# Kernel optimization log

Measured on AMD Instinct MI355X. Metric: run time of the kernel, lower is better.

## Reference

```python
import jax, jax.numpy as jnp
import numpy as np

DELAY = 4
SKIP = 2
NF = 8
HS = 256
EPS = 1e-5


def setup_inputs() -> dict:
    key = jax.random.key(0)
    ks = jax.random.split(key, 11)
    B, NP, NO, T = 16, 512, 512, 2048
    predictor = jax.random.normal(ks[0], (B, NP, T), dtype=jnp.float32)
    to_order = jax.random.normal(ks[1], (B, NO, T), dtype=jnp.float32)
    trilinear = jax.random.normal(ks[2], (NF, NO, NP), dtype=jnp.float32) / np.float32(np.sqrt(NP * NO))
    w_o = jax.random.normal(ks[3], (HS, NO), dtype=jnp.float32) / np.float32(np.sqrt(NO))
    b_o = jax.random.normal(ks[4], (HS,), dtype=jnp.float32) * 0.01
    w_p = jax.random.normal(ks[5], (HS, NP), dtype=jnp.float32) / np.float32(np.sqrt(NP))
    b_p = jax.random.normal(ks[6], (HS,), dtype=jnp.float32) * 0.01
    bn_gamma = jnp.ones((HS,), dtype=jnp.float32)
    bn_beta = jnp.zeros((HS,), dtype=jnp.float32)
    w_out = jax.random.normal(ks[7], (NF, HS), dtype=jnp.float32) / np.float32(np.sqrt(HS))
    b_out = jax.random.normal(ks[8], (NF,), dtype=jnp.float32) * 0.01
    return {"predictor": predictor, "to_order": to_order, "trilinear": trilinear,
            "w_o": w_o, "b_o": b_o, "w_p": w_p, "b_p": b_p,
            "bn_gamma": bn_gamma, "bn_beta": bn_beta, "w_out": w_out, "b_out": b_out}


def reference(predictor, to_order, trilinear, w_o, b_o, w_p, b_p, bn_gamma, bn_beta, w_out, b_out):
    B, NP, T = predictor.shape
    NO = to_order.shape[1]
    tot_latency = DELAY + SKIP * (NF - 1)
    T_r = T - tot_latency
    pred = predictor[:, :, :T_r]          # (B, np, Tr)
    too = to_order[:, :, DELAY:]          # (B, no, T - delay)
    # predictor_product[b,k,t,m] = sum_p pred[b,p,t] * trilinear[k,m,p]
    pp = jnp.einsum('bpt,kmp->bktm', pred, trilinear)           # (B, nf, Tr, no)
    win = jnp.stack([too[:, :, j * SKIP: j * SKIP + T_r] for j in range(NF)], axis=1)  # (B, nf, no, Tr)
    inner = jnp.einsum('bjmt,bktm->bjkt', win, pp)              # (B, nf, nf, Tr)
    # conv1d (kernel 1) heads
    o_proj = jnp.einsum('hm,bmt->bht', w_o, too) + b_o[None, :, None]    # (B, hs, T - delay)
    p_proj = jnp.einsum('hp,bpt->bht', w_p, pred) + b_p[None, :, None]   # (B, hs, Tr)
    o_win = jnp.stack([o_proj[:, :, j * SKIP: j * SKIP + T_r] for j in range(NF)], axis=1)  # (B, nf, hs, Tr)
    h = jax.nn.relu(o_win + p_proj[:, None])                    # (B, nf, hs, Tr)
    # BatchNorm1d (training-mode batch stats) over (B*nf, hs, Tr): stats over axes (0,1,3)
    mean = h.mean(axis=(0, 1, 3), keepdims=True)
    var = h.var(axis=(0, 1, 3), keepdims=True)
    h = (h - mean) * jax.lax.rsqrt(var + EPS) * bn_gamma[None, None, :, None] + bn_beta[None, None, :, None]
    head = jnp.einsum('kh,bjht->bjkt', w_out, h) + b_out[None, None, :, None]
    inner = inner + head
    log_probs = jax.nn.log_softmax(inner, axis=2)               # (B, nf, nf, Tr)
    correct = jnp.einsum('bjjt->bjt', log_probs)                # diagonal j == k
    return correct.mean(axis=2).mean(axis=0)                    # (nf,)
```

## Files before the change

### kernel.cpp

```cpp
#include <hip/hip_runtime.h>
#include <math.h>

constexpr int B_  = 16;
constexpr int NP_ = 512;
constexpr int NO_ = 512;
constexpr int T_  = 2048;
constexpr int NF_ = 8;
constexpr int HS_ = 256;
constexpr int TR_ = 2030;
constexpr int TO_ = 2044;
constexpr int OPLD_ = 2048;
constexpr float EPS_ = 1e-5f;

typedef short bf16x8 __attribute__((ext_vector_type(8)));
typedef float f32x16 __attribute__((ext_vector_type(16)));

__device__ __forceinline__ unsigned short f2bf(float f) {
  union { float f; unsigned int u; } v; v.f = f;
  unsigned int r = v.u + 0x7fffu + ((v.u >> 16) & 1u);
  return (unsigned short)(r >> 16);
}
__device__ __forceinline__ float bf2f(unsigned short u) {
  union { unsigned int u; float f; } v; v.u = ((unsigned int)u) << 16;
  return v.f;
}

typedef const __attribute__((address_space(1))) unsigned int* gas_u32;
typedef __attribute__((address_space(3))) unsigned int* las_u32;
__device__ __forceinline__ void gl16(const void* g, void* l) {
  __builtin_amdgcn_global_load_lds((gas_u32)g, (las_u32)l, 16, 0, 0);
}


__global__ __launch_bounds__(256) void transpose_cvt(
    const float* __restrict__ inA, unsigned short* __restrict__ outA,
    const float* __restrict__ inB, unsigned short* __restrict__ outB) {
  __shared__ float tile[64][65];
  const int c0 = blockIdx.x * 64;
  const int r0 = blockIdx.y * 64;
  const int z  = blockIdx.z;
  const int b  = z & 15;
  const float* ib = ((z < 16) ? inA : inB) + (size_t)b * 512 * 2048;
  unsigned short* ob = ((z < 16) ? outA : outB) + (size_t)b * 2048 * 512;
  for (int i = threadIdx.x; i < 64 * 16; i += 256) {
    const int r = i >> 4, c4 = (i & 15) * 4;
    float4 v = *(const float4*)(ib + (size_t)(r0 + r) * 2048 + c0 + c4);
    tile[r][c4 + 0] = v.x; tile[r][c4 + 1] = v.y;
    tile[r][c4 + 2] = v.z; tile[r][c4 + 3] = v.w;
  }
  __syncthreads();
  for (int i = threadIdx.x; i < 64 * 8; i += 256) {
    const int c = i >> 3, r8 = (i & 7) * 8;
    unsigned int pk[4];
    #pragma unroll
    for (int e = 0; e < 4; ++e)
      pk[e] = (unsigned int)f2bf(tile[r8 + 2 * e][c]) |
              ((unsigned int)f2bf(tile[r8 + 2 * e + 1][c]) << 16);
    *(uint4*)(ob + (size_t)(c0 + c) * 512 + r0 + r8) = *(uint4*)pk;
  }
}

__global__ __launch_bounds__(256) void cvt_all(
    const float* __restrict__ tri, unsigned short* __restrict__ trib,
    const float* __restrict__ wo, unsigned short* __restrict__ wob,
    const float* __restrict__ wp, unsigned short* __restrict__ wpb) {
  const int n1 = NF_ * NO_ * NP_, n2 = HS_ * 512;
  int i = (blockIdx.x * 256 + threadIdx.x) * 4;
  const float* in; unsigned short* out;
  if (i < n1)           { in = tri; out = trib; }
  else if (i < n1 + n2) { i -= n1; in = wo; out = wob; }
  else                  { i -= n1 + n2; in = wp; out = wpb; }
  float4 v = *(const float4*)(in + i);
  ushort4 o; o.x = f2bf(v.x); o.y = f2bf(v.y); o.z = f2bf(v.z); o.w = f2bf(v.w);
  *(ushort4*)(out + i) = o;
}

__global__ __launch_bounds__(256, 2) void proj_mfma(
    const unsigned short* __restrict__ Wo, const unsigned short* __restrict__ Wp,
    const unsigned short* __restrict__ Xo, const unsigned short* __restrict__ Xp,
    const float* __restrict__ biasO, const float* __restrict__ biasP,
    unsigned short* __restrict__ outO, unsigned short* __restrict__ outP) {
  __shared__ char smem[65536];
  char* const Ab[2] = { smem, smem + 16384 };
  char* const Bb[2] = { smem + 32768, smem + 49152 };
  const int sel = blockIdx.y >> 1;
  const unsigned short* Wbf = sel ? Wp : Wo;
  const unsigned short* Xt  = sel ? Xp : Xo;
  const float* bias = sel ? biasP : biasO;
  unsigned short* out = sel ? outP : outO;
  const int Tlen = sel ? TR_ : TO_;
  const int toff = sel ? 0 : 4;
  const int tid = threadIdx.x;
  const int l = tid & 63, wv = tid >> 6;
  const int h = l >> 5, tl = l & 31;
  const int mq = wv >> 1, tq = wv & 1;
  const int t0 = blockIdx.x * 128;
  const int m0 = (blockIdx.y & 1) * 128;
  const int b  = blockIdx.z;
  const unsigned short* Xb = Xt + (size_t)b * T_ * 512;

  int aSrc[4], bSrc[4], ldsO[4];
  #pragma unroll
  for (int i = 0; i < 4; ++i) {
    const int q = (wv << 8) + (i << 6) + l;
    const int r = q >> 3, c8s = (q & 7) ^ (r & 7);
    aSrc[i] = (m0 + r) * 512 + (c8s << 3);
    const int row = min(t0 + toff + r, T_ - 1);
    bSrc[i] = row * 512 + (c8s << 3);
    ldsO[i] = ((wv << 8) + (i << 6)) << 4;
  }

  f32x16 acc[2][2];
  #pragma unroll
  for (int i = 0; i < 2; ++i)
    #pragma unroll
    for (int jj = 0; jj < 2; ++jj)
      #pragma unroll
      for (int e = 0; e < 16; ++e) acc[i][jj][e] = 0.f;

  #pragma unroll
  for (int i = 0; i < 4; ++i) gl16(Wbf + aSrc[i], Ab[0] + ldsO[i]);
  #pragma unroll
  for (int i = 0; i < 4; ++i) gl16(Xb + bSrc[i], Bb[0] + ldsO[i]);
  asm volatile("s_waitcnt vmcnt(0)" ::: "memory");
  __builtin_amdgcn_s_barrier();

  #pragma unroll
  for (int ps = 0; ps < 8; ++ps) {
    const int cb = ps & 1;
    if (ps < 7) {
      const int p0 = (ps + 1) << 6;
      #pragma unroll
      for (int i = 0; i < 4; ++i) gl16(Wbf + p0 + aSrc[i], Ab[cb ^ 1] + ldsO[i]);
      #pragma unroll
      for (int i = 0; i < 4; ++i) gl16(Xb + p0 + bSrc[i], Bb[cb ^ 1] + ldsO[i]);
    }
    const unsigned short* As = (const unsigned short*)Ab[cb];
    const unsigned short* Bs = (const unsigned short*)Bb[cb];
    #pragma unroll
    for (int s = 0; s < 4; ++s) {
      const int k8 = 2 * s + h;
      bf16x8 af[2], bfr[2];
      #pragma unroll
      for (int mt = 0; mt < 2; ++mt) {
        const int rm = 64 * mq + 32 * mt + tl;
        af[mt] = *(const bf16x8*)(As + rm * 64 + ((k8 ^ (rm & 7)) << 3));
      }
      #pragma unroll
      for (int nt = 0; nt < 2; ++nt) {
        const int rt = 64 * tq + 32 * nt + tl;
        bfr[nt] = *(const bf16x8*)(Bs + rt * 64 + ((k8 ^ (rt & 7)) << 3));
      }
      #pragma unroll
      for (int mt = 0; mt < 2; ++mt)
        #pragma unroll
        for (int nt = 0; nt < 2; ++nt)
          acc[mt][nt] = __builtin_amdgcn_mfma_f32_32x32x16_bf16(
              af[mt], bfr[nt], acc[mt][nt], 0, 0, 0);
    }
    asm volatile("s_waitcnt vmcnt(0)" ::: "memory");
    __builtin_amdgcn_s_barrier();
  }
  #pragma unroll
  for (int mt = 0; mt < 2; ++mt)
    #pragma unroll
    for (int nt = 0; nt < 2; ++nt)
      #pragma unroll
      for (int r = 0; r < 16; ++r) {
        const int hs = m0 + 64 * mq + 32 * mt + (r & 3) + 8 * (r >> 2) + 4 * h;
        const int t  = t0 + 64 * tq + 32 * nt + tl;
        if (t < Tlen)
          out[((size_t)b * HS_ + hs) * OPLD_ + t] = f2bf(acc[mt][nt][r] + bias[hs]);
      }
}

__global__ __launch_bounds__(256, 2) void inner_mfma(
    const unsigned short* __restrict__ pred_t,
    const unsigned short* __restrict__ too_t,
    const unsigned short* __restrict__ tri_bf,
    float* __restrict__ inner) {
  __shared__ char smem[77824];
  char* const Pb[2] = { smem, smem + 16384 };
  char* const Tb[2] = { smem + 32768, smem + 49152 };
  char* const TOOM  = smem + 65536;
  char* const TAIL  = smem + 32768;
  const int tid = threadIdx.x;
  const int l = tid & 63, wv = tid >> 6;
  const int h = l >> 5, tl = l & 31;
  const int mh = wv & 1, th = wv >> 1;
  const int t0 = blockIdx.x * 128;
  const int kf0 = blockIdx.y * 2;
  const int b  = blockIdx.z;
  const unsigned short* predB = pred_t + (size_t)b * T_ * NP_;
  const unsigned short* tooB  = too_t  + (size_t)b * T_ * NO_;
  const unsigned short* triK  = tri_bf + (size_t)kf0 * NO_ * NP_;

  int pSrc[4], pLds[4];
  #pragma unroll
  for (int i = 0; i < 4; ++i) {
    const int q = (wv << 8) + (i << 6) + l;
    const int r = q >> 3, c8s = (q & 7) ^ (r & 7);
    pSrc[i] = (t0 + r) * NP_ + (c8s << 3);
    pLds[i] = ((wv << 8) + (i << 6)) << 4;
  }
  int tSrc[4], tLds[4];
  #pragma unroll
  for (int i = 0; i < 4; ++i) {
    const int q = (wv << 8) + (i << 6) + l;
    const int f = q >> 9, qq = q & 511;
    const int r = qq >> 3, c8s = (qq & 7) ^ (r & 7);
    tSrc[i] = f * (NO_ * NP_) + r * NP_ + (c8s << 3);
    tLds[i] = ((wv << 8) + (i << 6)) << 4;
  }
  int oSrc[3], oLds[3];
  #pragma unroll
  for (int i = 0; i < 3; ++i) {
    const int q = wv * 192 + (i << 6) + l;
    const int r = q >> 3, c8s = (q & 7) ^ (r & 7);
    oSrc[i] = (t0 + r) * NO_ + (c8s << 3);
    oLds[i] = (wv * 192 + (i << 6)) << 4;
  }
  int aSrcT[4], aLdsT[4];
  {
    const int ws = (wv >= 2) ? (wv - 2) : 0;
    #pragma unroll
    for (int i = 0; i < 4; ++i) {
      const int q = (ws << 8) + (i << 6) + l;
      const int r = 96 + (q >> 3), c8s = (q & 7) ^ (r & 7);
      aSrcT[i] = min(t0 + r, T_ - 1) * NO_ + (c8s << 3);
      aLdsT[i] = ((ws << 8) + (i << 6)) << 4;
    }
  }

  f32x16 Sacc[2][2];
  #pragma unroll
  for (int f = 0; f < 2; ++f)
    #pragma unroll
    for (int ct = 0; ct < 2; ++ct)
      #pragma unroll
      for (int e = 0; e < 16; ++e) Sacc[f][ct][e] = 0.f;

  for (int mc = 0; mc < 8; ++mc) {
    const int m0 = mc << 6;
    const int mOff = m0 * NP_;
    __builtin_amdgcn_s_barrier();
    #pragma unroll
    for (int i = 0; i < 3; ++i) gl16(tooB + m0 + oSrc[i], TOOM + oLds[i]);
    #pragma unroll
    for (int i = 0; i < 4; ++i) gl16(triK + mOff + tSrc[i], Tb[0] + tLds[i]);
    #pragma unroll
    for (int i = 0; i < 4; ++i) gl16(predB + pSrc[i], Pb[0] + pLds[i]);
    asm volatile("s_waitcnt vmcnt(0)" ::: "memory");
    __builtin_amdgcn_s_barrier();

    f32x16 Qacc[2][2];
    #pragma unroll
    for (int f = 0; f < 2; ++f)
      #pragma unroll
      for (int nt = 0; nt < 2; ++nt)
        #pragma unroll
        for (int e = 0; e < 16; ++e) Qacc[f][nt][e] = 0.f;

    #pragma unroll
    for (int ps = 0; ps < 8; ++ps) {
      const int cb = ps & 1;
      if (ps < 7) {
        const int p1 = (ps + 1) << 6;
        #pragma unroll
        for (int i = 0; i < 4; ++i)
          gl16(triK + mOff + p1 + tSrc[i], Tb[cb ^ 1] + tLds[i]);
        #pragma unroll
        for (int i = 0; i < 4; ++i)
          gl16(predB + p1 + pSrc[i], Pb[cb ^ 1] + pLds[i]);
      }
      const unsigned short* predS = (const unsigned short*)Pb[cb];
      const unsigned short* triS  = (const unsigned short*)Tb[cb];
      #pragma unroll
      for (int s = 0; s < 4; ++s) {
        const int k8 = 2 * s + h;
        const int swz = (k8 ^ (tl & 7)) << 3;
        bf16x8 a[2], bp[2];
        #pragma unroll
        for (int f = 0; f < 2; ++f)
          a[f] = *(const bf16x8*)(triS + f * 4096 + ((mh << 5) + tl) * 64 + swz);
        #pragma unroll
        for (int nt = 0; nt < 2; ++nt)
          bp[nt] = *(const bf16x8*)(predS + ((th << 6) + (nt << 5) + tl) * 64 + swz);
        #pragma unroll
        for (int f = 0; f < 2; ++f)
          #pragma unroll
          for (int nt = 0; nt < 2; ++nt)
            Qacc[f][nt] = __builtin_amdgcn_mfma_f32_32x32x16_bf16(
                a[f], bp[nt], Qacc[f][nt], 0, 0, 0);
      }
      if (ps == 7 && wv >= 2) {
        #pragma unroll
        for (int i = 0; i < 4; ++i)
          gl16(tooB + m0 + aSrcT[i], TAIL + aLdsT[i]);
      }
      asm volatile("s_waitcnt vmcnt(0)" ::: "memory");
      __builtin_amdgcn_s_barrier();
    }
    #pragma unroll
    for (int f = 0; f < 2; ++f)
      #pragma unroll
      for (int nt = 0; nt < 2; ++nt) {
        unsigned short* QSw = (unsigned short*)(Pb[f] + (((th << 1) + nt) << 12));
        #pragma unroll
        for (int rp = 0; rp < 8; ++rp) {
          const int r = rp << 1;
          const int m = (mh << 5) + (r & 3) + ((r >> 2) << 3) + (h << 2);
          const int c8 = m >> 3, ml = m & 7;
          const int rX = (tl & 24) | ((tl ^ c8) & 7);
          const unsigned int pk = (unsigned int)f2bf(Qacc[f][nt][r]) |
                                  ((unsigned int)f2bf(Qacc[f][nt][r + 1]) << 16);
          *(unsigned int*)(QSw + (((c8 << 5) + rX) << 3) + ml) = pk;
        }
      }
    asm volatile("s_waitcnt lgkmcnt(0)" ::: "memory");
    __builtin_amdgcn_s_barrier();
    #pragma unroll
    for (int s = 0; s < 4; ++s) {
      const int k8 = 2 * s + h;
      bf16x8 atoo[2];
      #pragma unroll
      for (int ct = 0; ct < 2; ++ct) {
        const int rbase = (wv + ct) << 5;
        const int rr = rbase + tl;
        const unsigned short* tb = (rbase < 96)
            ? (const unsigned short*)TOOM + (size_t)rr * 64
            : (const unsigned short*)TAIL + (size_t)(rr - 96) * 64;
        atoo[ct] = *(const bf16x8*)(tb + ((k8 ^ (rr & 7)) << 3));
      }
      const int rqX = (tl & 24) | ((tl ^ k8) & 7);
      #pragma unroll
      for (int f = 0; f < 2; ++f) {
        const bf16x8 bq = *(const bf16x8*)((const unsigned short*)(Pb[f] + (wv << 12)) +
                                           (((k8 << 5) + rqX) << 3));
        #pragma unroll
        for (int ct = 0; ct < 2; ++ct)
          Sacc[f][ct] = __builtin_amdgcn_mfma_f32_32x32x16_bf16(atoo[ct], bq, Sacc[f][ct], 0, 0, 0);
      }
    }
  }
  __syncthreads();
  const int tglob = t0 + (wv << 5) + tl;
  float* SW = (float*)smem + (wv << 11);
  #pragma unroll
  for (int f = 0; f < 2; ++f) {
    #pragma unroll
    for (int ct = 0; ct < 2; ++ct)
      #pragma unroll
      for (int r = 0; r < 16; ++r) {
        const int cc = (ct << 5) + (r & 3) + ((r >> 2) << 3) + (h << 2);
        SW[(cc << 5) + tl] = Sacc[f][ct][r];
      }
    if (tglob < TR_) {
      #pragma unroll
      for (int jj = 0; jj < 4; ++jj) {
        const int j = (jj << 1) + h;
        const float v = SW[((tl + 4 + 2 * j) << 5) + tl];
        inner[(((size_t)b * NF_ + j) * NF_ + (kf0 + f)) * TR_ + tglob] = v;
      }
    }
  }
}

__global__ __launch_bounds__(256) void bn_stats(
    const unsigned short* __restrict__ op, const unsigned short* __restrict__ pp,
    float* __restrict__ partials) {
  const int hh = blockIdx.x, b = blockIdx.y;
  const unsigned short* oprow = op + ((size_t)b * HS_ + hh) * OPLD_;
  const unsigned short* pprow = pp + ((size_t)b * HS_ + hh) * OPLD_;
  float s = 0.f, s2 = 0.f;
  const int t8 = threadIdx.x * 8;
  if (t8 < TR_) {
    uint4 pv4 = *(const uint4*)(pprow + t8);
    uint4 ov[3];
    ov[0] = *(const uint4*)(oprow + t8);
    ov[1] = *(const uint4*)(oprow + t8 + 8);
    ov[2] = *(const uint4*)(oprow + t8 + 16);
    float ppf[8], opf[24];
    #pragma unroll
    for (int i = 0; i < 4; ++i) {
      const unsigned int u = (&pv4.x)[i];
      ppf[2 * i]     = bf2f((unsigned short)(u & 0xffffu));
      ppf[2 * i + 1] = bf2f((unsigned short)(u >> 16));
    }
    #pragma unroll
    for (int g = 0; g < 3; ++g)
      #pragma unroll
      for (int i = 0; i < 4; ++i) {
        const unsigned int u = (&ov[g].x)[i];
        opf[8 * g + 2 * i]     = bf2f((unsigned short)(u & 0xffffu));
        opf[8 * g + 2 * i + 1] = bf2f((unsigned short)(u >> 16));
      }
    #pragma unroll
    for (int e = 0; e < 8; ++e) {
      if (t8 + e < TR_) {
        #pragma unroll
        for (int j = 0; j < NF_; ++j) {
          float r = fmaxf(opf[e + 2 * j] + ppf[e], 0.f);
          s += r; s2 += r * r;
        }
      }
    }
  }
  __shared__ float red[256], red2[256];
  red[threadIdx.x] = s; red2[threadIdx.x] = s2;
  __syncthreads();
  for (int st = 128; st > 0; st >>= 1) {
    if (threadIdx.x < st) {
      red[threadIdx.x]  += red[threadIdx.x + st];
      red2[threadIdx.x] += red2[threadIdx.x + st];
    }
    __syncthreads();
  }
  if (threadIdx.x == 0) {
    partials[b * HS_ + hh]            = red[0];
    partials[B_ * HS_ + b * HS_ + hh] = red2[0];
  }
}

__global__ __launch_bounds__(256) void bn_finalize(
    const float* __restrict__ partials, const float* __restrict__ gamma,
    const float* __restrict__ beta, const float* __restrict__ w_out,
    const float* __restrict__ b_out, float* __restrict__ w_eff,
    float* __restrict__ cvec) {
  const int hh = threadIdx.x;
  float s = 0.f, s2 = 0.f;
  for (int b = 0; b < B_; ++b) {
    s  += partials[b * HS_ + hh];
    s2 += partials[B_ * HS_ + b * HS_ + hh];
  }
  const float cnt  = (float)B_ * NF_ * TR_;
  const float mean = s / cnt;
  const float var  = s2 / cnt - mean * mean;
  const float scale = gamma[hh] * rsqrtf(var + EPS_);
  const float shift = beta[hh] - mean * scale;
  #pragma unroll
  for (int k = 0; k < NF_; ++k) w_eff[k * HS_ + hh] = w_out[k * HS_ + hh] * scale;
  __shared__ float red[256];
  for (int k = 0; k < NF_; ++k) {
    red[hh] = w_out[k * HS_ + hh] * shift;
    __syncthreads();
    for (int st = 128; st > 0; st >>= 1) {
      if (hh < st) red[hh] += red[hh + st];
      __syncthreads();
    }
    if (hh == 0) cvec[k] = b_out[k] + red[0];
    __syncthreads();
  }
}

__global__ __launch_bounds__(256) void head_final(
    const unsigned short* __restrict__ op, const unsigned short* __restrict__ pp,
    const float* __restrict__ w_eff, const float* __restrict__ cvec,
    const float* __restrict__ inner, float* __restrict__ part3) {
  __shared__ float opS[80 * 20];
  __shared__ float ppS[64 * 20];
  __shared__ float weS[8][256];
  __shared__ float red[4];
  const int tid = threadIdx.x;
  const int tl = tid & 63, jp = tid >> 6;
  const int t0 = blockIdx.x * 64;
  const int b  = blockIdx.y;
  const int jh = blockIdx.z;
  const int j  = (jh << 2) + jp;
  for (int i = tid; i < 8 * 256; i += 256) weS[i >> 8][i & 255] = w_eff[i];
  float acc[8] = {};
  const unsigned short* opb = op + (size_t)b * HS_ * OPLD_;
  const unsigned short* ppb = pp + (size_t)b * HS_ * OPLD_;
  for (int hc = 0; hc < 16; ++hc) {
    const int h0 = hc << 4;
    __syncthreads();
    if (tid < 160) {
      const int r = tid / 10, cc = (tid - r * 10) << 3;
      const int g = min(t0 + cc, OPLD_ - 8);
      uint4 v = *(const uint4*)(opb + (size_t)(h0 + r) * OPLD_ + g);
      #pragma unroll
      for (int e = 0; e < 4; ++e) {
        const unsigned int u = (&v.x)[e];
        opS[(cc + 2 * e) * 20 + r]     = bf2f((unsigned short)(u & 0xffffu));
        opS[(cc + 2 * e + 1) * 20 + r] = bf2f((unsigned short)(u >> 16));
      }
    }
    if (tid < 128) {
      const int r = tid >> 3, cc = (tid & 7) << 3;
      uint4 v = *(const uint4*)(ppb + (size_t)(h0 + r) * OPLD_ + t0 + cc);
      #pragma unroll
      for (int e = 0; e < 4; ++e) {
        const unsigned int u = (&v.x)[e];
        ppS[(cc + 2 * e) * 20 + r]     = bf2f((unsigned short)(u & 0xffffu));
        ppS[(cc + 2 * e + 1) * 20 + r] = bf2f((unsigned short)(u >> 16));
      }
    }
    __syncthreads();
    float pv[16];
    #pragma unroll
    for (int i = 0; i < 4; ++i) {
      float4 q = *(const float4*)(ppS + tl * 20 + 4 * i);
      pv[4 * i + 0] = q.x; pv[4 * i + 1] = q.y;
      pv[4 * i + 2] = q.z; pv[4 * i + 3] = q.w;
    }
    const int col = tl + 2 * j;
    #pragma unroll
    for (int i = 0; i < 4; ++i) {
      float4 ov = *(const float4*)(opS + col * 20 + 4 * i);
      #pragma unroll
      for (int e = 0; e < 4; ++e) {
        const float r = fmaxf((&ov.x)[e] + pv[4 * i + e], 0.f);
        #pragma unroll
        for (int k = 0; k < 8; ++k) acc[k] += weS[k][h0 + 4 * i + e] * r;
      }
    }
  }
  const int t = t0 + tl;
  float sj = 0.f;
  if (t < TR_) {
    float v[8]; float mx = -1e30f;
    #pragma unroll
    for (int k = 0; k < 8; ++k) {
      v[k] = acc[k] + cvec[k] +
             inner[(((size_t)b * NF_ + j) * NF_ + k) * TR_ + t];
      mx = fmaxf(mx, v[k]);
    }
    float se = 0.f;
    #pragma unroll
    for (int k = 0; k < 8; ++k) se += expf(v[k] - mx);
    sj = v[j] - mx - logf(se);
  }
  #pragma unroll
  for (int off = 32; off > 0; off >>= 1) sj += __shfl_down(sj, off);
  if ((tid & 63) == 0) red[jp] = sj;
  __syncthreads();
  if (tid < 4) {
    const int jw = (jh << 2) + tid;
    part3[(jw * B_ + b) * 32 + blockIdx.x] = red[tid];
  }
}

__global__ void final_out(const float* __restrict__ part3, float* __restrict__ out) {
  const int j = threadIdx.x;
  if (j < NF_) {
    float s = 0.f;
    for (int i = 0; i < B_ * 32; ++i) s += part3[j * B_ * 32 + i];
    out[j] = s / ((float)B_ * (float)TR_);
  }
}

extern "C" void kernel_launch(void* const* d_in, const int* in_sizes, int n_in,
                              void* d_out, int out_size, void* d_ws, size_t ws_size,
                              hipStream_t stream) {
  const float* predictor = (const float*)d_in[0];
  const float* to_order  = (const float*)d_in[1];
  const float* trilinear = (const float*)d_in[2];
  const float* w_o   = (const float*)d_in[3];
  const float* b_o   = (const float*)d_in[4];
  const float* w_p   = (const float*)d_in[5];
  const float* b_p   = (const float*)d_in[6];
  const float* bn_g  = (const float*)d_in[7];
  const float* bn_b  = (const float*)d_in[8];
  const float* w_out = (const float*)d_in[9];
  const float* b_out = (const float*)d_in[10];
  float* out = (float*)d_out;

  char* w = (char*)d_ws;
  unsigned short* pred_t = (unsigned short*)w; w += (size_t)B_ * T_ * NP_ * 2;
  unsigned short* too_t  = (unsigned short*)w; w += (size_t)B_ * T_ * NO_ * 2;
  unsigned short* tri_bf = (unsigned short*)w; w += (size_t)NF_ * NO_ * NP_ * 2;
  unsigned short* wo_bf  = (unsigned short*)w; w += (size_t)HS_ * NO_ * 2;
  unsigned short* wp_bf  = (unsigned short*)w; w += (size_t)HS_ * NP_ * 2;
  unsigned short* o_proj = (unsigned short*)w; w += (size_t)B_ * HS_ * OPLD_ * 2;
  unsigned short* p_proj = (unsigned short*)w; w += (size_t)B_ * HS_ * OPLD_ * 2;
  float* inner    = (float*)w; w += (size_t)B_ * NF_ * NF_ * TR_ * 4;
  float* partials = (float*)w; w += (size_t)2 * B_ * HS_ * 4;
  float* w_eff    = (float*)w; w += (size_t)NF_ * HS_ * 4;
  float* cvec     = (float*)w; w += 256;
  float* part3    = (float*)w; w += (size_t)NF_ * B_ * 32 * 4;

  transpose_cvt<<<dim3(32, 8, 32), 256, 0, stream>>>(predictor, pred_t,
                                                     to_order, too_t);
  cvt_all<<<2304, 256, 0, stream>>>(trilinear, tri_bf, w_o, wo_bf, w_p, wp_bf);

  proj_mfma<<<dim3(16, 4, 16), 256, 0, stream>>>(
      wo_bf, wp_bf, too_t, pred_t, b_o, b_p, o_proj, p_proj);

  inner_mfma<<<dim3(16, 4, 16), 256, 0, stream>>>(pred_t, too_t, tri_bf, inner);

  bn_stats<<<dim3(HS_, B_), 256, 0, stream>>>(o_proj, p_proj, partials);
  bn_finalize<<<1, 256, 0, stream>>>(partials, bn_g, bn_b, w_out, b_out, w_eff, cvec);
  head_final<<<dim3(32, B_, 2), 256, 0, stream>>>(o_proj, p_proj, w_eff, cvec, inner, part3);
  final_out<<<1, 64, 0, stream>>>(part3, out);
}
```

Baseline: 330.4 us.

## Triple-buffer predictor tiles and overlap to_order loads with inner MFMA loop

```diff
diff --git a/kernel.cpp b/kernel.cpp
--- a/kernel.cpp
+++ b/kernel.cpp
@@ -179,11 +179,7 @@
     const unsigned short* __restrict__ too_t,
     const unsigned short* __restrict__ tri_bf,
     float* __restrict__ inner) {
-  __shared__ char smem[77824];
-  char* const Pb[2] = { smem, smem + 16384 };
-  char* const Tb[2] = { smem + 32768, smem + 49152 };
-  char* const TOOM  = smem + 65536;
-  char* const TAIL  = smem + 32768;
+  __shared__ char smem[81920];
   const int tid = threadIdx.x;
   const int l = tid & 63, wv = tid >> 6;
   const int h = l >> 5, tl = l & 31;
@@ -212,24 +208,21 @@
     tSrc[i] = f * (NO_ * NP_) + r * NP_ + (c8s << 3);
     tLds[i] = ((wv << 8) + (i << 6)) << 4;
   }
-  int oSrc[3], oLds[3];
+  int oSrcM[2], oLdsM[2];
+  #pragma unroll
+  for (int i = 0; i < 2; ++i) {
+    const int q = (wv << 7) + (i << 6) + l;
+    const int r = q >> 3, c8s = (q & 7) ^ (r & 7);
+    oSrcM[i] = (t0 + r) * NO_ + (c8s << 3);
+    oLdsM[i] = q << 4;
+  }
+  int oSrcT[3], oLdsT[3];
   #pragma unroll
   for (int i = 0; i < 3; ++i) {
     const int q = wv * 192 + (i << 6) + l;
-    const int r = q >> 3, c8s = (q & 7) ^ (r & 7);
-    oSrc[i] = (t0 + r) * NO_ + (c8s << 3);
-    oLds[i] = (wv * 192 + (i << 6)) << 4;
-  }
-  int aSrcT[4], aLdsT[4];
-  {
-    const int ws = (wv >= 2) ? (wv - 2) : 0;
-    #pragma unroll
-    for (int i = 0; i < 4; ++i) {
-      const int q = (ws << 8) + (i << 6) + l;
-      const int r = 96 + (q >> 3), c8s = (q & 7) ^ (r & 7);
-      aSrcT[i] = min(t0 + r, T_ - 1) * NO_ + (c8s << 3);
-      aLdsT[i] = ((ws << 8) + (i << 6)) << 4;
-    }
+    const int rl = q >> 3, c8s = (q & 7) ^ (rl & 7);
+    oSrcT[i] = min(t0 + 64 + rl, T_ - 1) * NO_ + (c8s << 3);
+    oLdsT[i] = q << 4;
   }
 
   f32x16 Sacc[2][2];
@@ -245,13 +238,11 @@
     const int mOff = m0 * NP_;
     __builtin_amdgcn_s_barrier();
     #pragma unroll
-    for (int i = 0; i < 3; ++i) gl16(tooB + m0 + oSrc[i], TOOM + oLds[i]);
-    #pragma unroll
-    for (int i = 0; i < 4; ++i) gl16(triK + mOff + tSrc[i], Tb[0] + tLds[i]);
-    #pragma unroll
-    for (int i = 0; i < 4; ++i) gl16(predB + pSrc[i], Pb[0] + pLds[i]);
-    asm volatile("s_waitcnt vmcnt(0)" ::: "memory");
-    __builtin_amdgcn_s_barrier();
+    for (int i = 0; i < 4; ++i) gl16(triK + mOff + tSrc[i], smem + 49152 + tLds[i]);
+    #pragma unroll
+    for (int i = 0; i < 4; ++i) gl16(predB + pSrc[i], smem + pLds[i]);
+    #pragma unroll
+    for (int i = 0; i < 4; ++i) gl16(predB + 64 + pSrc[i], smem + 16384 + pLds[i]);
 
     f32x16 Qacc[2][2];
     #pragma unroll
@@ -263,18 +254,33 @@
 
     #pragma unroll
     for (int ps = 0; ps < 8; ++ps) {
-      const int cb = ps & 1;
+      if (ps < 7) asm volatile("s_waitcnt vmcnt(4)" ::: "memory");
+      else        asm volatile("s_waitcnt vmcnt(2)" ::: "memory");
+      __builtin_amdgcn_s_barrier();
       if (ps < 7) {
         const int p1 = (ps + 1) << 6;
-        #pragma unroll
-        for (int i = 0; i < 4; ++i)
-          gl16(triK + mOff + p1 + tSrc[i], Tb[cb ^ 1] + tLds[i]);
-        #pragma unroll
-        for (int i = 0; i < 4; ++i)
-          gl16(predB + p1 + pSrc[i], Pb[cb ^ 1] + pLds[i]);
-      }
-      const unsigned short* predS = (const unsigned short*)Pb[cb];
-      const unsigned short* triS  = (const unsigned short*)Tb[cb];
+        char* const tb1 = smem + 49152 + (((ps & 1) ^ 1) << 14);
+        #pragma unroll
+        for (int i = 0; i < 4; ++i) gl16(triK + mOff + p1 + tSrc[i], tb1 + tLds[i]);
+      }
+      if (ps < 6) {
+        const int p2 = (ps + 2) << 6;
+        char* const pb2 = smem + ((ps + 2) % 3) * 16384;
+        #pragma unroll
+        for (int i = 0; i < 4; ++i) gl16(predB + p2 + pSrc[i], pb2 + pLds[i]);
+      }
+      if (ps == 6) {
+        #pragma unroll
+        for (int i = 0; i < 2; ++i)
+          gl16(tooB + m0 + oSrcM[i], smem + 32768 + oLdsM[i]);
+      }
+      if (ps == 7) {
+        #pragma unroll
+        for (int i = 0; i < 3; ++i)
+          gl16(tooB + m0 + oSrcT[i], smem + 49152 + oLdsT[i]);
+      }
+      const unsigned short* predS = (const unsigned short*)(smem + (ps % 3) * 16384);
+      const unsigned short* triS  = (const unsigned short*)(smem + 49152 + ((ps & 1) << 14));
       #pragma unroll
       for (int s = 0; s < 4; ++s) {
         const int k8 = 2 * s + h;
@@ -293,19 +299,14 @@
             Qacc[f][nt] = __builtin_amdgcn_mfma_f32_32x32x16_bf16(
                 a[f], bp[nt], Qacc[f][nt], 0, 0, 0);
       }
-      if (ps == 7 && wv >= 2) {
-        #pragma unroll
-        for (int i = 0; i < 4; ++i)
-          gl16(tooB + m0 + aSrcT[i], TAIL + aLdsT[i]);
-      }
-      asm volatile("s_waitcnt vmcnt(0)" ::: "memory");
-      __builtin_amdgcn_s_barrier();
-    }
+    }
+    asm volatile("s_waitcnt vmcnt(0)" ::: "memory");
+    __builtin_amdgcn_s_barrier();
     #pragma unroll
     for (int f = 0; f < 2; ++f)
       #pragma unroll
       for (int nt = 0; nt < 2; ++nt) {
-        unsigned short* QSw = (unsigned short*)(Pb[f] + (((th << 1) + nt) << 12));
+        unsigned short* QSw = (unsigned short*)(smem + f * 16384 + (((th << 1) + nt) << 12));
         #pragma unroll
         for (int rp = 0; rp < 8; ++rp) {
           const int r = rp << 1;
@@ -327,16 +328,17 @@
       for (int ct = 0; ct < 2; ++ct) {
         const int rbase = (wv + ct) << 5;
         const int rr = rbase + tl;
-        const unsigned short* tb = (rbase < 96)
-            ? (const unsigned short*)TOOM + (size_t)rr * 64
-            : (const unsigned short*)TAIL + (size_t)(rr - 96) * 64;
+        const unsigned short* tb = (rbase < 64)
+            ? (const unsigned short*)(smem + 32768) + (size_t)rr * 64
+            : (const unsigned short*)(smem + 49152) + (size_t)(rr - 64) * 64;
         atoo[ct] = *(const bf16x8*)(tb + ((k8 ^ (rr & 7)) << 3));
       }
       const int rqX = (tl & 24) | ((tl ^ k8) & 7);
       #pragma unroll
       for (int f = 0; f < 2; ++f) {
-        const bf16x8 bq = *(const bf16x8*)((const unsigned short*)(Pb[f] + (wv << 12)) +
-                                           (((k8 << 5) + rqX) << 3));
+        const bf16x8 bq = *(const bf16x8*)(
+            (const unsigned short*)(smem + f * 16384 + (wv << 12)) +
+            (((k8 << 5) + rqX) << 3));
         #pragma unroll
         for (int ct = 0; ct < 2; ++ct)
           Sacc[f][ct] = __builtin_amdgcn_mfma_f32_32x32x16_bf16(atoo[ct], bq, Sacc[f][ct], 0, 0, 0);
```

New measurement: 333.6 us. Within noise of the previous version (+1.0%).
